# Kernel tuning notes

Hardware: AMD Instinct MI355X
Metric: run time of the kernel (lower is better)

## Reference

```python
import math
import jax
import jax.numpy as jnp
import numpy as np

KS = 7  # kernel_size


def _make_cdt_kernel():
    # kornia.create_meshgrid(k,k,normalized=False) -> coords; centered; hypot -> exp(d/-0.35)
    r = np.arange(KS, dtype=np.float32) - (KS // 2)
    yy, xx = np.meshgrid(r, r, indexing="ij")
    k = np.exp(np.hypot(xx, yy) / -0.35)
    return jnp.asarray(k, jnp.float32)[None, None]  # (1,1,KS,KS) OIHW


def setup_inputs() -> dict:
    key = jax.random.key(0)
    B, C, H, W = 32, 3, 256, 256
    u = jax.random.uniform(key, (B, C, H, W), dtype=jnp.float32)
    image = (u < 0.005).astype(jnp.float32)
    return {"image": image}


def reference(image):
    B, C, H, W = image.shape
    kernel = _make_cdt_kernel()
    n_iters = math.ceil(max(H, W) / (KS // 2))  # static
    x = image.reshape(B * C, 1, H, W)
    out0 = jnp.zeros_like(x)

    def step(carry, i):
        out, boundary = carry
        conv = jax.lax.conv_general_dilated(
            boundary, kernel, (1, 1), "SAME",
            dimension_numbers=("NCHW", "OIHW", "NCHW"))
        # -0.35*log(conv) with posinf (conv==0) replaced by 0, exactly as
        # torch.nan_to_num(cdt, posinf=0.0); safe-log form avoids inf/nan.
        pos = conv > 0
        cdt = jnp.where(pos, -0.35 * jnp.log(jnp.where(pos, conv, 1.0)), 0.0)
        mask = cdt > 0
        offset = i.astype(jnp.float32) * (KS / 2)  # i * kernel_size / 2 (true div)
        out = out + jnp.where(mask, offset + cdt, 0.0)
        boundary = jnp.where(mask, 1.0, boundary)
        return (out, boundary), None

    (out, _), _ = jax.lax.scan(step, (out0, x), jnp.arange(n_iters))
    return out.reshape(B, C, H, W)
```

## Files before the change

### kernel.cpp

```cpp
#include <hip/hip_runtime.h>


typedef unsigned short u16x4 __attribute__((ext_vector_type(4)));

#define BIGV (1 << 20)
#define ROWB 272
#define CHB (256 * ROWB)

__global__ __launch_bounds__(256) void k_rowdist(const float* __restrict__ img,
                                                 unsigned char* __restrict__ d1) {
  const int lane = threadIdx.x & 63;
  const int wv = threadIdx.x >> 6;
  const int row = blockIdx.x * 4 + wv;
  const int x0 = lane * 4;

  const float4 v = *reinterpret_cast<const float4*>(&img[(size_t)row * 256 + x0]);

  int c0 = (v.x != 0.0f) ? -x0 : BIGV;
  int c1 = (v.y != 0.0f) ? -(x0 + 1) : BIGV;
  int c2 = (v.z != 0.0f) ? -(x0 + 2) : BIGV;
  int c3 = (v.w != 0.0f) ? -(x0 + 3) : BIGV;
  const int p0 = c0;
  const int p1 = min(c1, p0);
  const int p2 = min(c2, p1);
  const int p3 = min(c3, p2);
  int incl = p3;
#pragma unroll
  for (int off = 1; off < 64; off <<= 1) {
    int o = __shfl_up(incl, off, 64);
    if (lane >= off) incl = min(incl, o);
  }
  int excl = __shfl_up(incl, 1, 64);
  if (lane == 0) excl = BIGV;
  const int df0 = x0 + min(p0, excl);
  const int df1 = x0 + 1 + min(p1, excl);
  const int df2 = x0 + 2 + min(p2, excl);
  const int df3 = x0 + 3 + min(p3, excl);

  int g0 = (v.x != 0.0f) ? x0 : BIGV;
  int g1 = (v.y != 0.0f) ? (x0 + 1) : BIGV;
  int g2 = (v.z != 0.0f) ? (x0 + 2) : BIGV;
  int g3 = (v.w != 0.0f) ? (x0 + 3) : BIGV;
  const int q3 = g3;
  const int q2 = min(g2, q3);
  const int q1 = min(g1, q2);
  const int q0 = min(g0, q1);
  int incl2 = q0;
#pragma unroll
  for (int off = 1; off < 64; off <<= 1) {
    int o = __shfl_down(incl2, off, 64);
    if (lane < 64 - off) incl2 = min(incl2, o);
  }
  int excl2 = __shfl_down(incl2, 1, 64);
  if (lane == 63) excl2 = BIGV;
  const int db0 = min(q0, excl2) - x0;
  const int db1 = min(q1, excl2) - (x0 + 1);
  const int db2 = min(q2, excl2) - (x0 + 2);
  const int db3 = min(q3, excl2) - (x0 + 3);

  const unsigned int d0 = (unsigned int)min(min(df0, db0), 127);
  const unsigned int d1v = (unsigned int)min(min(df1, db1), 127);
  const unsigned int d2 = (unsigned int)min(min(df2, db2), 127);
  const unsigned int d3 = (unsigned int)min(min(df3, db3), 127);
  const int ch = row >> 8, y = row & 255;
  const size_t base = (size_t)ch * CHB + (size_t)y * ROWB;
  *reinterpret_cast<unsigned int*>(&d1[base + 8 + x0]) =
      d0 | (d1v << 8) | (d2 << 16) | (d3 << 24);
  if (lane < 2)
    *reinterpret_cast<unsigned int*>(&d1[base + lane * 4]) = 0u;
  else if (lane >= 62)
    *reinterpret_cast<unsigned int*>(&d1[base + 264 + (lane - 62) * 4]) = 0u;
}

#define TAPROW(s_, t_, A0, A1, A2, A3, A4, A5, A6)                              \
  do {                                                                          \
    const unsigned int r0_ = R[(s_) + (t_)][0];                                 \
    const unsigned int r1_ = R[(s_) + (t_)][1];                                 \
    const unsigned int r2_ = R[(s_) + (t_)][2];                                 \
    A0 += (((__builtin_amdgcn_alignbyte(r1_, r0_, 1) + Cp) & 0x80808080u) >> 7);\
    A1 += (((__builtin_amdgcn_alignbyte(r1_, r0_, 2) + Cp) & 0x80808080u) >> 7);\
    A2 += (((__builtin_amdgcn_alignbyte(r1_, r0_, 3) + Cp) & 0x80808080u) >> 7);\
    A3 += (((r1_ + Cp) & 0x80808080u) >> 7);                                    \
    A4 += (((__builtin_amdgcn_alignbyte(r2_, r1_, 1) + Cp) & 0x80808080u) >> 7);\
    A5 += (((__builtin_amdgcn_alignbyte(r2_, r1_, 2) + Cp) & 0x80808080u) >> 7);\
    A6 += (((__builtin_amdgcn_alignbyte(r2_, r1_, 3) + Cp) & 0x80808080u) >> 7);\
  } while (0)

#define TAPROWC(s_, t_, A0, A1, A2, A4, A5, A6)                                 \
  do {                                                                          \
    const unsigned int r0_ = R[(s_) + (t_)][0];                                 \
    const unsigned int r1_ = R[(s_) + (t_)][1];                                 \
    const unsigned int r2_ = R[(s_) + (t_)][2];                                 \
    A0 += (((__builtin_amdgcn_alignbyte(r1_, r0_, 1) + Cp) & 0x80808080u) >> 7);\
    A1 += (((__builtin_amdgcn_alignbyte(r1_, r0_, 2) + Cp) & 0x80808080u) >> 7);\
    A2 += (((__builtin_amdgcn_alignbyte(r1_, r0_, 3) + Cp) & 0x80808080u) >> 7);\
    A4 += (((__builtin_amdgcn_alignbyte(r2_, r1_, 1) + Cp) & 0x80808080u) >> 7);\
    A5 += (((__builtin_amdgcn_alignbyte(r2_, r1_, 2) + Cp) & 0x80808080u) >> 7);\
    A6 += (((__builtin_amdgcn_alignbyte(r2_, r1_, 3) + Cp) & 0x80808080u) >> 7);\
  } while (0)

#define EPI(s_)                                                                 \
  do {                                                                          \
    const unsigned int Dc = R[(s_) + 3][1];                                     \
    const int d0_ = (int)(Dc & 255u);                                           \
    const int d1_ = (int)((Dc >> 8) & 255u);                                    \
    const int d2_ = (int)((Dc >> 16) & 255u);                                   \
    const int d3_ = (int)(Dc >> 24);                                            \
    const int i0_ = (max(d0_ - 1, 0) * 86) >> 8;                                \
    const int i1_ = (max(d1_ - 1, 0) * 86) >> 8;                                \
    const int i2_ = (max(d2_ - 1, 0) * 86) >> 8;                                \
    const int i3_ = (max(d3_ - 1, 0) * 86) >> 8;                                \
    const unsigned int Cp = (unsigned int)(127 - 3 * i0_) |                     \
                            ((unsigned int)(127 - 3 * i1_) << 8) |              \
                            ((unsigned int)(127 - 3 * i2_) << 16) |             \
                            ((unsigned int)(127 - 3 * i3_) << 24);              \
    unsigned int aA = 0, aB = 0, aC = 0, aD = 0;                                \
    TAPROW(s_, 0, aD, aD, aC, aC, aC, aD, aD);                                  \
    TAPROW(s_, 1, aD, aC, aB, aB, aB, aC, aD);                                  \
    TAPROW(s_, 2, aC, aB, aA, aA, aA, aB, aC);                                  \
    TAPROWC(s_, 3, aC, aB, aA, aA, aB, aC);                                     \
    TAPROW(s_, 4, aC, aB, aA, aA, aA, aB, aC);                                  \
    TAPROW(s_, 5, aD, aC, aB, aB, aB, aC, aD);                                  \
    TAPROW(s_, 6, aD, aD, aC, aC, aC, aD, aD);                                  \
    const float s0_ = fmaf((float)(aA & 255u), wA,                              \
                     fmaf((float)(aB & 255u), wB,                               \
                     fmaf((float)(aC & 255u), wC, (float)(aD & 255u) * wD)));   \
    const float s1f_ = fmaf((float)((aA >> 8) & 255u), wA,                      \
                      fmaf((float)((aB >> 8) & 255u), wB,                       \
                      fmaf((float)((aC >> 8) & 255u), wC,                       \
                           (float)((aD >> 8) & 255u) * wD)));                   \
    const float s2_ = fmaf((float)((aA >> 16) & 255u), wA,                      \
                     fmaf((float)((aB >> 16) & 255u), wB,                       \
                     fmaf((float)((aC >> 16) & 255u), wC,                       \
                          (float)((aD >> 16) & 255u) * wD)));                   \
    const float s3_ = fmaf((float)(aA >> 24), wA,                               \
                     fmaf((float)(aB >> 24), wB,                                \
                     fmaf((float)(aC >> 24), wC, (float)(aD >> 24) * wD)));     \
    const float cv0_ = W4 - s0_, cv1_ = W4 - s1f_;                              \
    const float cv2_ = W4 - s2_, cv3_ = W4 - s3_;                               \
    const float e0_ = fmaf(3.5f, (float)i0_, -0.35f * __logf(fmaxf(cv0_, 1e-30f))); \
    const float e1_ = fmaf(3.5f, (float)i1_, -0.35f * __logf(fmaxf(cv1_, 1e-30f))); \
    const float e2_ = fmaf(3.5f, (float)i2_, -0.35f * __logf(fmaxf(cv2_, 1e-30f))); \
    const float e3_ = fmaf(3.5f, (float)i3_, -0.35f * __logf(fmaxf(cv3_, 1e-30f))); \
    const float4 o4_ = make_float4(                                             \
        (d0_ > 0 && cv0_ > 1e-6f) ? e0_ : 0.0f,                                 \
        (d1_ > 0 && cv1_ > 1e-6f) ? e1_ : 0.0f,                                 \
        (d2_ > 0 && cv2_ > 1e-6f) ? e2_ : 0.0f,                                 \
        (d3_ > 0 && cv3_ > 1e-6f) ? e3_ : 0.0f);                                \
    *reinterpret_cast<float4*>(&out[obase + (size_t)(s_) * 256]) = o4_;         \
  } while (0)

#define LDQ(off) (*reinterpret_cast<const u16x4*>(&s1[(off)]))
#define EMIN __builtin_elementwise_min
#define EMAX __builtin_elementwise_max

#define PFX(OUT, a0, a1, a2, a3, a4, a5, a6, a7, a8, a9, a10, a11, a12, a13,    \
            a14, a15, a16)                                                      \
  u16x4 OUT = EMIN(                                                             \
      EMIN(EMIN(EMIN(EMAX(a7, K1), EMAX(a9, K1)),                               \
                EMIN(EMAX(a6, K2), EMAX(a10, K2))),                             \
           EMIN(EMIN(EMAX(a5, K3), EMAX(a11, K3)),                              \
                EMIN(EMAX(a4, K4), EMAX(a12, K4)))),                            \
      EMIN(EMIN(EMIN(EMAX(a3, K5), EMAX(a13, K5)),                              \
                EMIN(EMAX(a2, K6), EMAX(a14, K6))),                             \
           EMIN(EMIN(EMAX(a1, K7), EMAX(a15, K7)),                              \
                EMIN(EMAX(a0, K8), EMAX(a16, K8)))));                           \
  OUT = EMIN(OUT, a8)

#define TUP(OUT, b3, b2, b1, b0, d0, d1, d2, d3)                                \
  OUT = EMIN(OUT, EMIN(EMIN(EMIN(EMAX(b3, Kc0), EMAX(b2, Kc1)),                 \
                            EMIN(EMAX(b1, Kc2), EMAX(b0, Kc3))),                \
                       EMIN(EMIN(EMAX(d0, Kc0), EMAX(d1, Kc1)),                 \
                            EMIN(EMAX(d2, Kc2), EMAX(d3, Kc3)))))

#define BMOF(MX)                                                                \
  ({                                                                            \
    const unsigned long long mb_ = __builtin_bit_cast(unsigned long long, MX);  \
    const unsigned int ml_ = (unsigned int)mb_, mh_ = (unsigned int)(mb_ >> 32);\
    max(max((int)(ml_ & 0xFFFFu), (int)(ml_ >> 16)),                            \
        max((int)(mh_ & 0xFFFFu), (int)(mh_ >> 16)));                           \
  })

__global__ __launch_bounds__(256) void k_fused(const unsigned char* __restrict__ d1,
                                               float* __restrict__ out) {
  const int ch = blockIdx.z;
  const int yt = blockIdx.y;
  const int xt = blockIdx.x;
  const int x0 = xt * 32;
  const int y0 = yt * 128;
  const int tid = threadIdx.x;
  const int lastxt = (int)gridDim.x - 1;

  __shared__ __align__(16) unsigned char s1[279 * 96];
  __shared__ __align__(16) unsigned char Ds[136 * 44];

  for (int i = tid; i < 552; i += 256) {
    const int r = (i * 2731) >> 16;
    const int c = i - r * 24;
    const int row = (r < 11) ? r : r + 256;
    *reinterpret_cast<unsigned int*>(&s1[row * 96 + c * 4]) = 0x007F007Fu;
  }
  const unsigned char* src = d1 + (size_t)ch * CHB + x0;
#pragma unroll
  for (int it = 0; it < 3; ++it) {
    const int idx = it * 256 + tid;
    const int y = (idx * 21846) >> 16;
    const int seg = idx - y * 3;
    const uint4 q = *reinterpret_cast<const uint4*>(&src[y * ROWB + seg * 16]);
    uint4 lo, hi;
    lo.x = __builtin_amdgcn_perm(0u, q.x, 0x0C010C00u);
    lo.y = __builtin_amdgcn_perm(0u, q.x, 0x0C030C02u);
    lo.z = __builtin_amdgcn_perm(0u, q.y, 0x0C010C00u);
    lo.w = __builtin_amdgcn_perm(0u, q.y, 0x0C030C02u);
    hi.x = __builtin_amdgcn_perm(0u, q.z, 0x0C010C00u);
    hi.y = __builtin_amdgcn_perm(0u, q.z, 0x0C030C02u);
    hi.z = __builtin_amdgcn_perm(0u, q.w, 0x0C010C00u);
    hi.w = __builtin_amdgcn_perm(0u, q.w, 0x0C030C02u);
    *reinterpret_cast<uint4*>(&s1[(y + 11) * 96 + seg * 32]) = lo;
    *reinterpret_cast<uint4*>(&s1[(y + 11) * 96 + seg * 32 + 16]) = hi;
  }
  __syncthreads();

  const u16x4 K1 = {1, 1, 1, 1}, K2 = {2, 2, 2, 2}, K3 = {3, 3, 3, 3},
              K4 = {4, 4, 4, 4}, K5 = {5, 5, 5, 5}, K6 = {6, 6, 6, 6},
              K7 = {7, 7, 7, 7}, K8 = {8, 8, 8, 8};
#pragma unroll 1
  for (int t = tid; t < 270; t += 256) {
    const int rg5 = (t * 6554) >> 16;
    const int g = t - rg5 * 10;
    const int r0r = rg5 * 5;
    const int ybase = y0 + r0r - 3;
    const int dsb = r0r * 44 + g * 4;
    if ((xt == 0 && g == 0) || (xt == lastxt && g == 9)) {
      *reinterpret_cast<unsigned int*>(&Ds[dsb]) = 0x7F7F7F7Fu;
      *reinterpret_cast<unsigned int*>(&Ds[dsb + 44]) = 0x7F7F7F7Fu;
      *reinterpret_cast<unsigned int*>(&Ds[dsb + 88]) = 0x7F7F7F7Fu;
      *reinterpret_cast<unsigned int*>(&Ds[dsb + 132]) = 0x7F7F7F7Fu;
      *reinterpret_cast<unsigned int*>(&Ds[dsb + 176]) = 0x7F7F7F7Fu;
      continue;
    }
    const int jb = 8 + 8 * g;
    const int ab = (ybase + 3) * 96 + jb;
    const u16x4 w0 = LDQ(ab), w1 = LDQ(ab + 96), w2 = LDQ(ab + 192),
                w3 = LDQ(ab + 288), w4 = LDQ(ab + 384), w5 = LDQ(ab + 480),
                w6 = LDQ(ab + 576), w7 = LDQ(ab + 672), w8 = LDQ(ab + 768),
                w9 = LDQ(ab + 864), w10 = LDQ(ab + 960), w11 = LDQ(ab + 1056),
                w12 = LDQ(ab + 1152), w13 = LDQ(ab + 1248), w14 = LDQ(ab + 1344),
                w15 = LDQ(ab + 1440), w16 = LDQ(ab + 1536), w17 = LDQ(ab + 1632),
                w18 = LDQ(ab + 1728), w19 = LDQ(ab + 1824), w20 = LDQ(ab + 1920);
    PFX(o0, w0, w1, w2, w3, w4, w5, w6, w7, w8, w9, w10, w11, w12, w13, w14, w15, w16);
    PFX(o1, w1, w2, w3, w4, w5, w6, w7, w8, w9, w10, w11, w12, w13, w14, w15, w16, w17);
    PFX(o2, w2, w3, w4, w5, w6, w7, w8, w9, w10, w11, w12, w13, w14, w15, w16, w17, w18);
    PFX(o3, w3, w4, w5, w6, w7, w8, w9, w10, w11, w12, w13, w14, w15, w16, w17, w18, w19);
    PFX(o4, w4, w5, w6, w7, w8, w9, w10, w11, w12, w13, w14, w15, w16, w17, w18, w19, w20);
    u16x4 mx = EMAX(EMAX(o0, o1), EMAX(EMAX(o2, o3), o4));
    int bm = BMOF(mx);
    int kc = 9;
    while (kc < bm) {
      const unsigned short q0 = (unsigned short)kc, q1 = (unsigned short)(kc + 1),
                           q2 = (unsigned short)(kc + 2), q3 = (unsigned short)(kc + 3);
      const u16x4 Kc0 = {q0, q0, q0, q0}, Kc1 = {q1, q1, q1, q1},
                  Kc2 = {q2, q2, q2, q2}, Kc3 = {q3, q3, q3, q3};
      const int lo = jb, hi = 278 * 96 + jb;
      const int aup = (ybase - kc + 8) * 96 + jb;
      const int adn = (ybase + kc + 11) * 96 + jb;
      const u16x4 t0 = LDQ(max(aup, lo)), t1 = LDQ(max(aup + 96, lo)),
                  t2 = LDQ(max(aup + 192, lo)), t3 = LDQ(max(aup + 288, lo)),
                  t4 = LDQ(max(aup + 384, lo)), t5 = LDQ(max(aup + 480, lo)),
                  t6 = LDQ(max(aup + 576, lo)), t7 = LDQ(max(aup + 672, lo));
      const u16x4 u0 = LDQ(min(adn, hi)), u1 = LDQ(min(adn + 96, hi)),
                  u2 = LDQ(min(adn + 192, hi)), u3 = LDQ(min(adn + 288, hi)),
                  u4 = LDQ(min(adn + 384, hi)), u5 = LDQ(min(adn + 480, hi)),
                  u6 = LDQ(min(adn + 576, hi)), u7 = LDQ(min(adn + 672, hi));
      TUP(o0, t3, t2, t1, t0, u0, u1, u2, u3);
      TUP(o1, t4, t3, t2, t1, u1, u2, u3, u4);
      TUP(o2, t5, t4, t3, t2, u2, u3, u4, u5);
      TUP(o3, t6, t5, t4, t3, u3, u4, u5, u6);
      TUP(o4, t7, t6, t5, t4, u4, u5, u6, u7);
      kc += 4;
      mx = EMAX(EMAX(o0, o1), EMAX(EMAX(o2, o3), o4));
      bm = BMOF(mx);
    }
#define STROW(j_, OJ)                                                           \
    {                                                                           \
      const unsigned long long ob = __builtin_bit_cast(unsigned long long, OJ); \
      unsigned int packed = __builtin_amdgcn_perm(                              \
          (unsigned int)(ob >> 32), (unsigned int)ob, 0x06040200u);             \
      if ((unsigned int)(ybase + (j_)) > 255u) packed = 0x7F7F7F7Fu;            \
      *reinterpret_cast<unsigned int*>(&Ds[dsb + (j_) * 44]) = packed;          \
    }
    STROW(0, o0); STROW(1, o1); STROW(2, o2); STROW(3, o3); STROW(4, o4);
#undef STROW
  }
  __syncthreads();

  const float wA = 3.17814e-2f, wB = 2.35426e-3f, wC = 1.91126e-4f, wD = 1.35150e-5f;
  const float W4 = 8.0f * wA + 12.0f * wB + 16.0f * wC + 12.0f * wD;

  const int cg = tid & 7;
  const int rg = tid >> 3;
  const int rl0 = rg * 4;
  const int jb2 = cg * 4;
  const size_t obase = (size_t)ch * 65536 + (size_t)(y0 + rl0) * 256 + x0 + cg * 4;

  unsigned int R[10][3];
#pragma unroll
  for (int u = 0; u < 10; ++u) {
    const unsigned char* p = &Ds[(rl0 + u) * 44 + jb2];
    R[u][0] = *reinterpret_cast<const unsigned int*>(p);
    R[u][1] = *reinterpret_cast<const unsigned int*>(p + 4);
    R[u][2] = *reinterpret_cast<const unsigned int*>(p + 8);
  }

  EPI(0); EPI(1); EPI(2); EPI(3);
}

extern "C" void kernel_launch(void* const* d_in, const int* in_sizes, int n_in,
                              void* d_out, int out_size, void* d_ws, size_t ws_size,
                              hipStream_t stream) {
  const float* img = (const float*)d_in[0];
  float* out = (float*)d_out;
  unsigned char* Dbuf = (unsigned char*)d_ws;

  const int total = in_sizes[0];
  const int nch = total >> 16;

  k_rowdist<<<dim3(nch * 64), dim3(256), 0, stream>>>(img, Dbuf);
  k_fused<<<dim3(8, 2, nch), dim3(256), 0, stream>>>(Dbuf, out);
}
```

Before: 46.44 us.

## Split fused column-distance pass into separate kernel writing distances to global

Moves the column-wise distance propagation out of the fused kernel into a new k_coldist kernel that covers 16-column strips and writes a full byte distance map to workspace. The final kernel then just loads its haloed tile of distances and runs the epilogue. This removes the redundant column computation on halo rows and columns that each fused tile used to repeat, and lowers shared memory per block. In exchange it adds a third launch and a global round trip for the distance map.

```diff
diff --git a/kernel.cpp b/kernel.cpp
--- a/kernel.cpp
+++ b/kernel.cpp
@@ -70,6 +70,127 @@
     *reinterpret_cast<unsigned int*>(&d1[base + lane * 4]) = 0u;
   else if (lane >= 62)
     *reinterpret_cast<unsigned int*>(&d1[base + 264 + (lane - 62) * 4]) = 0u;
+}
+
+#define LDQ(off) (*reinterpret_cast<const u16x4*>(&s1[(off)]))
+#define EMIN __builtin_elementwise_min
+#define EMAX __builtin_elementwise_max
+
+#define PFX(OUT, a0, a1, a2, a3, a4, a5, a6, a7, a8, a9, a10, a11, a12, a13,    \
+            a14, a15, a16)                                                      \
+  u16x4 OUT = EMIN(                                                             \
+      EMIN(EMIN(EMIN(EMAX(a7, K1), EMAX(a9, K1)),                               \
+                EMIN(EMAX(a6, K2), EMAX(a10, K2))),                             \
+           EMIN(EMIN(EMAX(a5, K3), EMAX(a11, K3)),                              \
+                EMIN(EMAX(a4, K4), EMAX(a12, K4)))),                            \
+      EMIN(EMIN(EMIN(EMAX(a3, K5), EMAX(a13, K5)),                              \
+                EMIN(EMAX(a2, K6), EMAX(a14, K6))),                             \
+           EMIN(EMIN(EMAX(a1, K7), EMAX(a15, K7)),                              \
+                EMIN(EMAX(a0, K8), EMAX(a16, K8)))));                           \
+  OUT = EMIN(OUT, a8)
+
+#define TUP(OUT, b3, b2, b1, b0, d0, d1, d2, d3)                                \
+  OUT = EMIN(OUT, EMIN(EMIN(EMIN(EMAX(b3, Kc0), EMAX(b2, Kc1)),                 \
+                            EMIN(EMAX(b1, Kc2), EMAX(b0, Kc3))),                \
+                       EMIN(EMIN(EMAX(d0, Kc0), EMAX(d1, Kc1)),                 \
+                            EMIN(EMAX(d2, Kc2), EMAX(d3, Kc3)))))
+
+#define BMOF(MX)                                                                \
+  ({                                                                            \
+    const unsigned long long mb_ = __builtin_bit_cast(unsigned long long, MX);  \
+    const unsigned int ml_ = (unsigned int)mb_, mh_ = (unsigned int)(mb_ >> 32);\
+    max(max((int)(ml_ & 0xFFFFu), (int)(ml_ >> 16)),                            \
+        max((int)(mh_ & 0xFFFFu), (int)(mh_ >> 16)));                           \
+  })
+
+__global__ __launch_bounds__(256) void k_coldist(const unsigned char* __restrict__ d1,
+                                                 unsigned char* __restrict__ Dg) {
+  const int ch = blockIdx.y;
+  const int xt = blockIdx.x;
+  const int x0 = xt * 16;
+  const int tid = threadIdx.x;
+
+  __shared__ __align__(16) unsigned char s1[279 * 40];
+
+  if (tid < 230) {
+    const int r = (tid * 6554) >> 16;
+    const int c = tid - r * 10;
+    const int row = (r < 11) ? r : r + 256;
+    *reinterpret_cast<unsigned int*>(&s1[row * 40 + c * 4]) = 0x007F007Fu;
+  }
+  const unsigned char* src = d1 + (size_t)ch * CHB + 8 + x0;
+#pragma unroll
+  for (int it = 0; it < 4; ++it) {
+    const int idx = it * 256 + tid;
+    const int y = idx >> 2, c = idx & 3;
+    const unsigned int q = *reinterpret_cast<const unsigned int*>(&src[y * ROWB + c * 4]);
+    *reinterpret_cast<unsigned int*>(&s1[(y + 11) * 40 + c * 8]) =
+        __builtin_amdgcn_perm(0u, q, 0x0C010C00u);
+    *reinterpret_cast<unsigned int*>(&s1[(y + 11) * 40 + c * 8 + 4]) =
+        __builtin_amdgcn_perm(0u, q, 0x0C030C02u);
+  }
+  __syncthreads();
+
+  if (tid < 208) {
+    const u16x4 K1 = {1, 1, 1, 1}, K2 = {2, 2, 2, 2}, K3 = {3, 3, 3, 3},
+                K4 = {4, 4, 4, 4}, K5 = {5, 5, 5, 5}, K6 = {6, 6, 6, 6},
+                K7 = {7, 7, 7, 7}, K8 = {8, 8, 8, 8};
+    const int rg = tid >> 2;
+    const int g = tid & 3;
+    const int ybase = rg * 5;
+    const int jb = g * 8;
+    const int ab = (ybase + 3) * 40 + jb;
+    const u16x4 w0 = LDQ(ab), w1 = LDQ(ab + 40), w2 = LDQ(ab + 80),
+                w3 = LDQ(ab + 120), w4 = LDQ(ab + 160), w5 = LDQ(ab + 200),
+                w6 = LDQ(ab + 240), w7 = LDQ(ab + 280), w8 = LDQ(ab + 320),
+                w9 = LDQ(ab + 360), w10 = LDQ(ab + 400), w11 = LDQ(ab + 440),
+                w12 = LDQ(ab + 480), w13 = LDQ(ab + 520), w14 = LDQ(ab + 560),
+                w15 = LDQ(ab + 600), w16 = LDQ(ab + 640), w17 = LDQ(ab + 680),
+                w18 = LDQ(ab + 720), w19 = LDQ(ab + 760), w20 = LDQ(ab + 800);
+    PFX(o0, w0, w1, w2, w3, w4, w5, w6, w7, w8, w9, w10, w11, w12, w13, w14, w15, w16);
+    PFX(o1, w1, w2, w3, w4, w5, w6, w7, w8, w9, w10, w11, w12, w13, w14, w15, w16, w17);
+    PFX(o2, w2, w3, w4, w5, w6, w7, w8, w9, w10, w11, w12, w13, w14, w15, w16, w17, w18);
+    PFX(o3, w3, w4, w5, w6, w7, w8, w9, w10, w11, w12, w13, w14, w15, w16, w17, w18, w19);
+    PFX(o4, w4, w5, w6, w7, w8, w9, w10, w11, w12, w13, w14, w15, w16, w17, w18, w19, w20);
+    u16x4 mx = EMAX(EMAX(o0, o1), EMAX(EMAX(o2, o3), o4));
+    int bm = BMOF(mx);
+    int kc = 9;
+    while (kc < bm) {
+      const unsigned short q0 = (unsigned short)kc, q1 = (unsigned short)(kc + 1),
+                           q2 = (unsigned short)(kc + 2), q3 = (unsigned short)(kc + 3);
+      const u16x4 Kc0 = {q0, q0, q0, q0}, Kc1 = {q1, q1, q1, q1},
+                  Kc2 = {q2, q2, q2, q2}, Kc3 = {q3, q3, q3, q3};
+      const int lo2 = jb, hi2 = 278 * 40 + jb;
+      const int aup = (ybase - kc + 8) * 40 + jb;
+      const int adn = (ybase + kc + 11) * 40 + jb;
+      const u16x4 t0 = LDQ(max(aup, lo2)), t1 = LDQ(max(aup + 40, lo2)),
+                  t2 = LDQ(max(aup + 80, lo2)), t3 = LDQ(max(aup + 120, lo2)),
+                  t4 = LDQ(max(aup + 160, lo2)), t5 = LDQ(max(aup + 200, lo2)),
+                  t6 = LDQ(max(aup + 240, lo2)), t7 = LDQ(max(aup + 280, lo2));
+      const u16x4 u0 = LDQ(min(adn, hi2)), u1 = LDQ(min(adn + 40, hi2)),
+                  u2 = LDQ(min(adn + 80, hi2)), u3 = LDQ(min(adn + 120, hi2)),
+                  u4 = LDQ(min(adn + 160, hi2)), u5 = LDQ(min(adn + 200, hi2)),
+                  u6 = LDQ(min(adn + 240, hi2)), u7 = LDQ(min(adn + 280, hi2));
+      TUP(o0, t3, t2, t1, t0, u0, u1, u2, u3);
+      TUP(o1, t4, t3, t2, t1, u1, u2, u3, u4);
+      TUP(o2, t5, t4, t3, t2, u2, u3, u4, u5);
+      TUP(o3, t6, t5, t4, t3, u3, u4, u5, u6);
+      TUP(o4, t7, t6, t5, t4, u4, u5, u6, u7);
+      kc += 4;
+      mx = EMAX(EMAX(o0, o1), EMAX(EMAX(o2, o3), o4));
+      bm = BMOF(mx);
+    }
+    const size_t Db = (size_t)ch * 65536 + (size_t)ybase * 256 + x0 + g * 4;
+#define STROW(j_, OJ)                                                           \
+    if (ybase + (j_) <= 255) {                                                  \
+      const unsigned long long ob = __builtin_bit_cast(unsigned long long, OJ); \
+      *reinterpret_cast<unsigned int*>(&Dg[Db + (size_t)(j_) * 256]) =          \
+          __builtin_amdgcn_perm((unsigned int)(ob >> 32), (unsigned int)ob,     \
+                                0x06040200u);                                   \
+    }
+    STROW(0, o0) STROW(1, o1) STROW(2, o2) STROW(3, o3) STROW(4, o4)
+#undef STROW
+  }
 }
 
 #define TAPROW(s_, t_, A0, A1, A2, A3, A4, A5, A6)                              \
@@ -150,38 +271,7 @@
     *reinterpret_cast<float4*>(&out[obase + (size_t)(s_) * 256]) = o4_;         \
   } while (0)
 
-#define LDQ(off) (*reinterpret_cast<const u16x4*>(&s1[(off)]))
-#define EMIN __builtin_elementwise_min
-#define EMAX __builtin_elementwise_max
-
-#define PFX(OUT, a0, a1, a2, a3, a4, a5, a6, a7, a8, a9, a10, a11, a12, a13,    \
-            a14, a15, a16)                                                      \
-  u16x4 OUT = EMIN(                                                             \
-      EMIN(EMIN(EMIN(EMAX(a7, K1), EMAX(a9, K1)),                               \
-                EMIN(EMAX(a6, K2), EMAX(a10, K2))),                             \
-           EMIN(EMIN(EMAX(a5, K3), EMAX(a11, K3)),                              \
-                EMIN(EMAX(a4, K4), EMAX(a12, K4)))),                            \
-      EMIN(EMIN(EMIN(EMAX(a3, K5), EMAX(a13, K5)),                              \
-                EMIN(EMAX(a2, K6), EMAX(a14, K6))),                             \
-           EMIN(EMIN(EMAX(a1, K7), EMAX(a15, K7)),                              \
-                EMIN(EMAX(a0, K8), EMAX(a16, K8)))));                           \
-  OUT = EMIN(OUT, a8)
-
-#define TUP(OUT, b3, b2, b1, b0, d0, d1, d2, d3)                                \
-  OUT = EMIN(OUT, EMIN(EMIN(EMIN(EMAX(b3, Kc0), EMAX(b2, Kc1)),                 \
-                            EMIN(EMAX(b1, Kc2), EMAX(b0, Kc3))),                \
-                       EMIN(EMIN(EMAX(d0, Kc0), EMAX(d1, Kc1)),                 \
-                            EMIN(EMAX(d2, Kc2), EMAX(d3, Kc3)))))
-
-#define BMOF(MX)                                                                \
-  ({                                                                            \
-    const unsigned long long mb_ = __builtin_bit_cast(unsigned long long, MX);  \
-    const unsigned int ml_ = (unsigned int)mb_, mh_ = (unsigned int)(mb_ >> 32);\
-    max(max((int)(ml_ & 0xFFFFu), (int)(ml_ >> 16)),                            \
-        max((int)(mh_ & 0xFFFFu), (int)(mh_ >> 16)));                           \
-  })
-
-__global__ __launch_bounds__(256) void k_fused(const unsigned char* __restrict__ d1,
+__global__ __launch_bounds__(256) void k_final(const unsigned char* __restrict__ Dg,
                                                float* __restrict__ out) {
   const int ch = blockIdx.z;
   const int yt = blockIdx.y;
@@ -189,108 +279,23 @@
   const int x0 = xt * 32;
   const int y0 = yt * 128;
   const int tid = threadIdx.x;
-  const int lastxt = (int)gridDim.x - 1;
-
-  __shared__ __align__(16) unsigned char s1[279 * 96];
-  __shared__ __align__(16) unsigned char Ds[136 * 44];
-
-  for (int i = tid; i < 552; i += 256) {
-    const int r = (i * 2731) >> 16;
-    const int c = i - r * 24;
-    const int row = (r < 11) ? r : r + 256;
-    *reinterpret_cast<unsigned int*>(&s1[row * 96 + c * 4]) = 0x007F007Fu;
-  }
-  const unsigned char* src = d1 + (size_t)ch * CHB + x0;
-#pragma unroll
-  for (int it = 0; it < 3; ++it) {
+
+  __shared__ __align__(16) unsigned char Ds[134 * 44];
+
+  const unsigned char* Dc0 = Dg + (size_t)ch * 65536;
+#pragma unroll
+  for (int it = 0; it < 6; ++it) {
     const int idx = it * 256 + tid;
-    const int y = (idx * 21846) >> 16;
-    const int seg = idx - y * 3;
-    const uint4 q = *reinterpret_cast<const uint4*>(&src[y * ROWB + seg * 16]);
-    uint4 lo, hi;
-    lo.x = __builtin_amdgcn_perm(0u, q.x, 0x0C010C00u);
-    lo.y = __builtin_amdgcn_perm(0u, q.x, 0x0C030C02u);
-    lo.z = __builtin_amdgcn_perm(0u, q.y, 0x0C010C00u);
-    lo.w = __builtin_amdgcn_perm(0u, q.y, 0x0C030C02u);
-    hi.x = __builtin_amdgcn_perm(0u, q.z, 0x0C010C00u);
-    hi.y = __builtin_amdgcn_perm(0u, q.z, 0x0C030C02u);
-    hi.z = __builtin_amdgcn_perm(0u, q.w, 0x0C010C00u);
-    hi.w = __builtin_amdgcn_perm(0u, q.w, 0x0C030C02u);
-    *reinterpret_cast<uint4*>(&s1[(y + 11) * 96 + seg * 32]) = lo;
-    *reinterpret_cast<uint4*>(&s1[(y + 11) * 96 + seg * 32 + 16]) = hi;
-  }
-  __syncthreads();
-
-  const u16x4 K1 = {1, 1, 1, 1}, K2 = {2, 2, 2, 2}, K3 = {3, 3, 3, 3},
-              K4 = {4, 4, 4, 4}, K5 = {5, 5, 5, 5}, K6 = {6, 6, 6, 6},
-              K7 = {7, 7, 7, 7}, K8 = {8, 8, 8, 8};
-#pragma unroll 1
-  for (int t = tid; t < 270; t += 256) {
-    const int rg5 = (t * 6554) >> 16;
-    const int g = t - rg5 * 10;
-    const int r0r = rg5 * 5;
-    const int ybase = y0 + r0r - 3;
-    const int dsb = r0r * 44 + g * 4;
-    if ((xt == 0 && g == 0) || (xt == lastxt && g == 9)) {
-      *reinterpret_cast<unsigned int*>(&Ds[dsb]) = 0x7F7F7F7Fu;
-      *reinterpret_cast<unsigned int*>(&Ds[dsb + 44]) = 0x7F7F7F7Fu;
-      *reinterpret_cast<unsigned int*>(&Ds[dsb + 88]) = 0x7F7F7F7Fu;
-      *reinterpret_cast<unsigned int*>(&Ds[dsb + 132]) = 0x7F7F7F7Fu;
-      *reinterpret_cast<unsigned int*>(&Ds[dsb + 176]) = 0x7F7F7F7Fu;
-      continue;
+    if (idx < 1340) {
+      const int r = (idx * 6554) >> 16;
+      const int c = idx - r * 10;
+      const int y = y0 - 3 + r;
+      const int xc = x0 - 4 + c * 4;
+      unsigned int v = 0x7F7F7F7Fu;
+      if ((unsigned int)y < 256u && (unsigned int)xc < 256u)
+        v = *reinterpret_cast<const unsigned int*>(&Dc0[(size_t)y * 256 + xc]);
+      *reinterpret_cast<unsigned int*>(&Ds[r * 44 + c * 4]) = v;
     }
-    const int jb = 8 + 8 * g;
-    const int ab = (ybase + 3) * 96 + jb;
-    const u16x4 w0 = LDQ(ab), w1 = LDQ(ab + 96), w2 = LDQ(ab + 192),
-                w3 = LDQ(ab + 288), w4 = LDQ(ab + 384), w5 = LDQ(ab + 480),
-                w6 = LDQ(ab + 576), w7 = LDQ(ab + 672), w8 = LDQ(ab + 768),
-                w9 = LDQ(ab + 864), w10 = LDQ(ab + 960), w11 = LDQ(ab + 1056),
-                w12 = LDQ(ab + 1152), w13 = LDQ(ab + 1248), w14 = LDQ(ab + 1344),
-                w15 = LDQ(ab + 1440), w16 = LDQ(ab + 1536), w17 = LDQ(ab + 1632),
-                w18 = LDQ(ab + 1728), w19 = LDQ(ab + 1824), w20 = LDQ(ab + 1920);
-    PFX(o0, w0, w1, w2, w3, w4, w5, w6, w7, w8, w9, w10, w11, w12, w13, w14, w15, w16);
-    PFX(o1, w1, w2, w3, w4, w5, w6, w7, w8, w9, w10, w11, w12, w13, w14, w15, w16, w17);
-    PFX(o2, w2, w3, w4, w5, w6, w7, w8, w9, w10, w11, w12, w13, w14, w15, w16, w17, w18);
-    PFX(o3, w3, w4, w5, w6, w7, w8, w9, w10, w11, w12, w13, w14, w15, w16, w17, w18, w19);
-    PFX(o4, w4, w5, w6, w7, w8, w9, w10, w11, w12, w13, w14, w15, w16, w17, w18, w19, w20);
-    u16x4 mx = EMAX(EMAX(o0, o1), EMAX(EMAX(o2, o3), o4));
-    int bm = BMOF(mx);
-    int kc = 9;
-    while (kc < bm) {
-      const unsigned short q0 = (unsigned short)kc, q1 = (unsigned short)(kc + 1),
-                           q2 = (unsigned short)(kc + 2), q3 = (unsigned short)(kc + 3);
-      const u16x4 Kc0 = {q0, q0, q0, q0}, Kc1 = {q1, q1, q1, q1},
-                  Kc2 = {q2, q2, q2, q2}, Kc3 = {q3, q3, q3, q3};
-      const int lo = jb, hi = 278 * 96 + jb;
-      const int aup = (ybase - kc + 8) * 96 + jb;
-      const int adn = (ybase + kc + 11) * 96 + jb;
-      const u16x4 t0 = LDQ(max(aup, lo)), t1 = LDQ(max(aup + 96, lo)),
-                  t2 = LDQ(max(aup + 192, lo)), t3 = LDQ(max(aup + 288, lo)),
-                  t4 = LDQ(max(aup + 384, lo)), t5 = LDQ(max(aup + 480, lo)),
-                  t6 = LDQ(max(aup + 576, lo)), t7 = LDQ(max(aup + 672, lo));
-      const u16x4 u0 = LDQ(min(adn, hi)), u1 = LDQ(min(adn + 96, hi)),
-                  u2 = LDQ(min(adn + 192, hi)), u3 = LDQ(min(adn + 288, hi)),
-                  u4 = LDQ(min(adn + 384, hi)), u5 = LDQ(min(adn + 480, hi)),
-                  u6 = LDQ(min(adn + 576, hi)), u7 = LDQ(min(adn + 672, hi));
-      TUP(o0, t3, t2, t1, t0, u0, u1, u2, u3);
-      TUP(o1, t4, t3, t2, t1, u1, u2, u3, u4);
-      TUP(o2, t5, t4, t3, t2, u2, u3, u4, u5);
-      TUP(o3, t6, t5, t4, t3, u3, u4, u5, u6);
-      TUP(o4, t7, t6, t5, t4, u4, u5, u6, u7);
-      kc += 4;
-      mx = EMAX(EMAX(o0, o1), EMAX(EMAX(o2, o3), o4));
-      bm = BMOF(mx);
-    }
-#define STROW(j_, OJ)                                                           \
-    {                                                                           \
-      const unsigned long long ob = __builtin_bit_cast(unsigned long long, OJ); \
-      unsigned int packed = __builtin_amdgcn_perm(                              \
-          (unsigned int)(ob >> 32), (unsigned int)ob, 0x06040200u);             \
-      if ((unsigned int)(ybase + (j_)) > 255u) packed = 0x7F7F7F7Fu;            \
-      *reinterpret_cast<unsigned int*>(&Ds[dsb + (j_) * 44]) = packed;          \
-    }
-    STROW(0, o0); STROW(1, o1); STROW(2, o2); STROW(3, o3); STROW(4, o4);
-#undef STROW
   }
   __syncthreads();
 
@@ -324,7 +329,9 @@
 
   const int total = in_sizes[0];
   const int nch = total >> 16;
+  unsigned char* Dmat = Dbuf + (size_t)nch * CHB;
 
   k_rowdist<<<dim3(nch * 64), dim3(256), 0, stream>>>(img, Dbuf);
-  k_fused<<<dim3(8, 2, nch), dim3(256), 0, stream>>>(Dbuf, out);
+  k_coldist<<<dim3(16, nch), dim3(256), 0, stream>>>(Dbuf, Dmat);
+  k_final<<<dim3(8, 2, nch), dim3(256), 0, stream>>>(Dmat, out);
 }
```

Result: slower. 51.26 us (+10.4%).
